# Kernel tuning notes

Measured on AMD Instinct MI355X. Metric: run time of the kernel, lower is better.

Reference implementation:

```python
import jax, jax.numpy as jnp
import numpy as np

NC = 10      # num_classes
HID = 64     # hidden_layer_dim
CIN = 512    # input_channels
THRESH = 100 # _LABEL2MASK_THRESHOL


def setup_inputs() -> dict:
    key = jax.random.key(0)
    k = jax.random.split(key, 5)
    B, h, w = 4, 60, 80
    feature1 = jax.random.normal(k[0], (B, CIN, h, w), jnp.float32)
    feature2 = jax.random.normal(k[1], (B, CIN, h // 2, w // 2), jnp.float32)
    s_in = (2.0 / CIN) ** 0.5   # kaiming_normal_ fan_in for 1x1 conv
    s_h = (2.0 / HID) ** 0.5
    w1 = jax.random.normal(k[2], (HID, CIN), jnp.float32) * s_in
    b1 = jnp.zeros((HID,), jnp.float32)
    w2 = jax.random.normal(k[3], (HID, CIN), jnp.float32) * s_in
    b2 = jnp.zeros((HID,), jnp.float32)
    w3 = jax.random.normal(k[4], (NC + 1, HID), jnp.float32) * s_h
    b3 = jnp.zeros((NC + 1,), jnp.float32)
    return {"feature1": feature1, "feature2": feature2,
            "w1": w1, "b1": b1, "w2": w2, "b2": b2, "w3": w3, "b3": b3}


def _resize_bilinear(x, H, W):
    # torch nn.Upsample(mode='bilinear', align_corners=False) ~ jax.image.resize bilinear
    B, C = x.shape[0], x.shape[1]
    return jax.image.resize(x, (B, C, H, W), method="bilinear")


def _label2bbx(seg):
    # Vectorized replacement of the batch x class Python loop: fused masked
    # min/max reductions per (batch, class). Classes 1..NC-1, class 0 skipped,
    # exactly as in the original. Fixed output shape (B*(NC-1), 6); rows with
    # pixel count < THRESH are filled with -1 (jit-compatible padding).
    B, H, W = seg.shape
    cls = jnp.arange(1, NC)                                   # (NC-1,)
    mask = seg[:, None, :, :] == cls[None, :, None, None]     # (B, NC-1, H, W)
    xs = jnp.arange(W)
    ys = jnp.arange(H)
    count = mask.sum(axis=(-2, -1))                           # (B, NC-1)
    xmin = jnp.min(jnp.where(mask, xs[None, None, None, :], W), axis=(-2, -1))
    xmax = jnp.max(jnp.where(mask, xs[None, None, None, :], -1), axis=(-2, -1))
    ymin = jnp.min(jnp.where(mask, ys[None, None, :, None], H), axis=(-2, -1))
    ymax = jnp.max(jnp.where(mask, ys[None, None, :, None], -1), axis=(-2, -1))
    bids = jnp.broadcast_to(jnp.arange(B)[:, None], (B, NC - 1))
    clsb = jnp.broadcast_to(cls[None, :], (B, NC - 1))
    bbx = jnp.stack([bids, xmin, ymin, xmax, ymax, clsb], axis=-1)  # (B, NC-1, 6)
    valid = (count >= THRESH)[..., None]
    return jnp.where(valid, bbx, -1).reshape(B * (NC - 1), 6)


def reference(feature1, feature2, w1, b1, w2, b2, w3, b3):
    # 1x1 convs expressed as channel GEMMs
    f1 = jax.nn.relu(jnp.einsum('bchw,oc->bohw', feature1, w1) + b1[None, :, None, None])
    f2 = jax.nn.relu(jnp.einsum('bchw,oc->bohw', feature2, w2) + b2[None, :, None, None])
    h, w = feature1.shape[2], feature1.shape[3]
    f2 = _resize_bilinear(f2, h, w)           # Upsample x2
    inter = f1 + f2
    up = _resize_bilinear(inter, 8 * h, 8 * w)  # Upsample x8
    logits = jax.nn.relu(jnp.einsum('bchw,oc->bohw', up, w3) + b3[None, :, None, None])
    probability = jax.nn.softmax(logits, axis=1)   # Softmax2d = softmax over C
    segmentation = jnp.argmax(probability, axis=1)  # (B, H, W)
    bbx = _label2bbx(segmentation)
    return probability, segmentation, bbx
```

## Files before the change

### kernel.cpp

```cpp
#include <hip/hip_runtime.h>

#define DEVINL __device__ __forceinline__

namespace {

constexpr int NB   = 4;
constexpr int CINv = 512;
constexpr int HIDv = 64;
constexpr int NCl  = 11;
constexpr int h1v = 60, w1v = 80;
constexpr int h2v = 30, w2v = 40;
constexpr int Hf = 480, Wf = 640;
constexpr int PPB1 = h1v * w1v;
constexpr int PPB2 = h2v * w2v;
constexpr int NP1 = NB * PPB1;
constexpr int NP2 = NB * PPB2;
constexpr int PPBF = Hf * Wf;
constexpr int NPF = NB * PPBF;

constexpr size_t WS_P1  = 0;
constexpr size_t WS_P2  = WS_P1 + 2ull * HIDv * NP1;
constexpr size_t WS_Z   = WS_P2 + 2ull * HIDv * NP2;
constexpr size_t WS_BBX = WS_Z + (size_t)NB * NCl * PPB1;

constexpr size_t OUT_SEG = (size_t)NB * NCl * PPBF;
constexpr size_t OUT_BBX = OUT_SEG + (size_t)NPF;

DEVINL int iclamp(int v, int lo, int hi) { return v < lo ? lo : (v > hi ? hi : v); }

template <int PPB>
DEVINL void gemm_tile(const float* __restrict__ F, const float* __restrict__ Wt,
                      float* __restrict__ P, int npix, int tile, int khalf,
                      float* A_lds , float* W_lds ) {
  const int t = threadIdx.x;
  const int pg = t & 15;
  const int og = t >> 4;
  const int gp0 = tile * 64;
  const int c0 = khalf * 256;

  float acc[4][4];
#pragma unroll
  for (int i = 0; i < 4; ++i)
#pragma unroll
    for (int j = 0; j < 4; ++j) acc[i][j] = 0.f;

  for (int kb = 0; kb < 8; ++kb) {
    const int cb = c0 + kb * 32;
    __syncthreads();
#pragma unroll
    for (int e = 0; e < 8; ++e) {
      int idx = e * 256 + t;
      int cc = idx >> 6, px = idx & 63;
      int gp = gp0 + px;
      int b = gp / PPB, pb = gp % PPB;
      A_lds[idx] = F[((size_t)b * CINv + (cb + cc)) * PPB + pb];
    }
#pragma unroll
    for (int e = 0; e < 8; ++e) {
      int idx = e * 256 + t;
      int o = idx >> 5, cc = idx & 31;
      W_lds[cc * 68 + o] = Wt[o * CINv + cb + cc];
    }
    __syncthreads();
#pragma unroll
    for (int cc = 0; cc < 32; ++cc) {
      float4 a = *reinterpret_cast<const float4*>(&A_lds[cc * 64 + pg * 4]);
      float4 w = *reinterpret_cast<const float4*>(&W_lds[cc * 68 + og * 4]);
      float av[4] = {a.x, a.y, a.z, a.w};
      float wv[4] = {w.x, w.y, w.z, w.w};
#pragma unroll
      for (int i = 0; i < 4; ++i)
#pragma unroll
        for (int j = 0; j < 4; ++j)
          acc[i][j] = fmaf(av[i], wv[j], acc[i][j]);
    }
  }
#pragma unroll
  for (int j = 0; j < 4; ++j) {
    int o = og * 4 + j;
    float4 v;
    v.x = acc[0][j]; v.y = acc[1][j]; v.z = acc[2][j]; v.w = acc[3][j];
    *reinterpret_cast<float4*>(&P[((size_t)khalf * HIDv + o) * npix + gp0 + pg * 4]) = v;
  }
}

__global__ __launch_bounds__(256) void k_gemm(const float* __restrict__ f1,
                                              const float* __restrict__ f2,
                                              const float* __restrict__ w1,
                                              const float* __restrict__ w2,
                                              float* __restrict__ ws) {
  __shared__ float A_lds[32 * 64];
  __shared__ float W_lds[32 * 68];
  const int bid = blockIdx.x;

  if (bid == 0 && threadIdx.x < 180) {
    int f = threadIdx.x % 5;
    int v = (f == 0) ? 0 : ((f == 1 || f == 3) ? 0x7fffffff : (int)0x80000000);
    reinterpret_cast<int*>(ws + WS_BBX)[threadIdx.x] = v;
  }

  if (bid < 600) {
    gemm_tile<PPB1>(f1, w1, ws + WS_P1, NP1, bid >> 1, bid & 1, A_lds, W_lds);
  } else {
    int tt = bid - 600;
    gemm_tile<PPB2>(f2, w2, ws + WS_P2, NP2, tt >> 1, tt & 1, A_lds, W_lds);
  }
}

__global__ __launch_bounds__(256) void k_combine_z(const float* __restrict__ ws_ro,
                                                   float* __restrict__ ws,
                                                   const float* __restrict__ b1,
                                                   const float* __restrict__ b2,
                                                   const float* __restrict__ w3,
                                                   const float* __restrict__ b3) {
  __shared__ float inter[64 * 64];
  const int t = threadIdx.x;
  const int pxl = t & 63;
  const int qi = t >> 6;
  const int gp = blockIdx.x * 64 + pxl;
  const int b = gp / PPB1, pb = gp % PPB1;
  const int y = pb / w1v, x = pb % w1v;

  const float sx = x * 0.5f - 0.25f;
  const float x0f = floorf(sx);
  const float fx = sx - x0f;
  const int ix0 = iclamp((int)x0f, 0, w2v - 1);
  const int ix1 = iclamp((int)x0f + 1, 0, w2v - 1);
  const float sy = y * 0.5f - 0.25f;
  const float y0f = floorf(sy);
  const float fy = sy - y0f;
  const int iy0 = iclamp((int)y0f, 0, h2v - 1);
  const int iy1 = iclamp((int)y0f + 1, 0, h2v - 1);

  const float* p1 = ws_ro + WS_P1;
  const float* p2 = ws_ro + WS_P2;
  const int base2 = b * PPB2;
  const int i00 = base2 + iy0 * w2v + ix0;
  const int i01 = base2 + iy0 * w2v + ix1;
  const int i10 = base2 + iy1 * w2v + ix0;
  const int i11 = base2 + iy1 * w2v + ix1;

#pragma unroll
  for (int cc = 0; cc < 16; ++cc) {
    const int ch = qi * 16 + cc;
    float v = p1[(size_t)ch * NP1 + gp] + p1[(size_t)(HIDv + ch) * NP1 + gp] + b1[ch];
    v = fmaxf(v, 0.f);
    const float* pa = p2 + (size_t)ch * NP2;
    const float* pbp = p2 + (size_t)(HIDv + ch) * NP2;
    const float bb = b2[ch];
    float v00 = fmaxf(pa[i00] + pbp[i00] + bb, 0.f);
    float v01 = fmaxf(pa[i01] + pbp[i01] + bb, 0.f);
    float v10 = fmaxf(pa[i10] + pbp[i10] + bb, 0.f);
    float v11 = fmaxf(pa[i11] + pbp[i11] + bb, 0.f);
    float top = v00 + fx * (v01 - v00);
    float bot = v10 + fx * (v11 - v10);
    v += top + fy * (bot - top);
    inter[ch * 64 + pxl] = v;
  }
  __syncthreads();

  const int o0 = qi * 3;
  const int ocnt = (qi == 3) ? 2 : 3;
  float* z = ws + WS_Z;
  for (int oo = 0; oo < ocnt; ++oo) {
    const int o = o0 + oo;
    float acc = b3[o];
#pragma unroll
    for (int ch = 0; ch < 64; ++ch)
      acc = fmaf(inter[ch * 64 + pxl], w3[o * HIDv + ch], acc);
    z[((size_t)b * NCl + o) * PPB1 + pb] = acc;
  }
}

__global__ __launch_bounds__(256) void k_up_softmax(const float* __restrict__ ws,
                                                    float* __restrict__ out,
                                                    int* __restrict__ bbxAcc) {
  constexpr int ZR = 3, ZC = 18, ZN = NCl * ZR * ZC;
  __shared__ float zt[ZN];
  __shared__ int sCnt[10], sXmin[10], sXmax[10], sYmin[10], sYmax[10];

  const int t = threadIdx.x;
  const int tile = blockIdx.x;
  const int tx = tile % 5;
  const int ty = (tile / 5) % 60;
  const int b  = tile / 300;

  const int base_x = tx * 16 - 1;
  const int base_y = ty - 1;

  if (t < 10) {
    sCnt[t] = 0;
    sXmin[t] = 0x7fffffff; sXmax[t] = (int)0x80000000;
    sYmin[t] = 0x7fffffff; sYmax[t] = (int)0x80000000;
  }
  const float* zb = ws + WS_Z + (size_t)b * NCl * PPB1;
  for (int e = t; e < ZN; e += 256) {
    int ch = e / (ZR * ZC);
    int rc = e % (ZR * ZC);
    int row = rc / ZC, col = rc % ZC;
    int gr = iclamp(base_y + row, 0, h1v - 1);
    int gc = iclamp(base_x + col, 0, w1v - 1);
    zt[e] = zb[(size_t)ch * PPB1 + gr * w1v + gc];
  }
  __syncthreads();

  const int xg = t & 31;
  const int yr = t >> 5;
  const int X = tx * 128 + xg * 4;
  const int Y = ty * 8 + yr;
  const int r = Y * Wf + X;

  const int lcx0 = (xg + 1) >> 1;
  const int lry0 = (yr >= 4) ? 1 : 0;
  const float fy = (Y + 0.5f) * 0.125f - 0.5f - (float)(base_y + lry0);
  float fxk[4];
#pragma unroll
  for (int k = 0; k < 4; ++k)
    fxk[k] = (X + k + 0.5f) * 0.125f - 0.5f - (float)(base_x + lcx0);

  float lg[NCl][4];
#pragma unroll
  for (int c = 0; c < NCl; ++c) {
    const int base = c * (ZR * ZC) + lry0 * ZC + lcx0;
    float v00 = zt[base],       v01 = zt[base + 1];
    float v10 = zt[base + ZC],  v11 = zt[base + ZC + 1];
    float l0 = v00 + fy * (v10 - v00);
    float l1 = v01 + fy * (v11 - v01);
#pragma unroll
    for (int k = 0; k < 4; ++k)
      lg[c][k] = fmaxf(l0 + fxk[k] * (l1 - l0), 0.f);
  }

  int bestc[4];
#pragma unroll
  for (int k = 0; k < 4; ++k) {
    float m = lg[0][k];
    int bi = 0;
#pragma unroll
    for (int c = 1; c < NCl; ++c) {
      if (lg[c][k] > m) { m = lg[c][k]; bi = c; }
    }
    bestc[k] = bi;
    float s = 0.f;
#pragma unroll
    for (int c = 0; c < NCl; ++c) {
      float e = __expf(lg[c][k] - m);
      lg[c][k] = e;
      s += e;
    }
    const float inv = __builtin_amdgcn_rcpf(s);
#pragma unroll
    for (int c = 0; c < NCl; ++c) lg[c][k] *= inv;
  }

  float* prob = out + (size_t)b * NCl * PPBF;
#pragma unroll
  for (int c = 0; c < NCl; ++c) {
    float4 v;
    v.x = lg[c][0]; v.y = lg[c][1]; v.z = lg[c][2]; v.w = lg[c][3];
    *reinterpret_cast<float4*>(&prob[(size_t)c * PPBF + r]) = v;
  }
  {
    float4 v;
    v.x = (float)bestc[0]; v.y = (float)bestc[1];
    v.z = (float)bestc[2]; v.w = (float)bestc[3];
    *reinterpret_cast<float4*>(&out[OUT_SEG + (size_t)b * PPBF + r]) = v;
  }

  for (int c = 1; c <= 9; ++c) {
    int cnt = 0, mnx = 0x7fffffff, mxx = (int)0x80000000;
#pragma unroll
    for (int k = 0; k < 4; ++k)
      if (bestc[k] == c) { ++cnt; mnx = min(mnx, X + k); mxx = max(mxx, X + k); }
    if (cnt) {
      atomicAdd(&sCnt[c], cnt);
      atomicMin(&sXmin[c], mnx);
      atomicMax(&sXmax[c], mxx);
      atomicMin(&sYmin[c], Y);
      atomicMax(&sYmax[c], Y);
    }
  }
  __syncthreads();
  if (t >= 1 && t <= 9 && sCnt[t] > 0) {
    int* e = bbxAcc + (b * 9 + (t - 1)) * 5;
    atomicAdd(e + 0, sCnt[t]);
    atomicMin(e + 1, sXmin[t]);
    atomicMax(e + 2, sXmax[t]);
    atomicMin(e + 3, sYmin[t]);
    atomicMax(e + 4, sYmax[t]);
  }
}

__global__ void k_bbx_final(const int* __restrict__ acc, float* __restrict__ out) {
  const int t = threadIdx.x;
  if (t >= 36) return;
  const int* e = acc + t * 5;
  float* o = out + OUT_BBX + t * 6;
  if (e[0] >= 100) {
    o[0] = (float)(t / 9);
    o[1] = (float)e[1];
    o[2] = (float)e[3];
    o[3] = (float)e[2];
    o[4] = (float)e[4];
    o[5] = (float)(t % 9 + 1);
  } else {
    for (int i = 0; i < 6; ++i) o[i] = -1.f;
  }
}

}

extern "C" void kernel_launch(void* const* d_in, const int* in_sizes, int n_in,
                              void* d_out, int out_size, void* d_ws, size_t ws_size,
                              hipStream_t stream) {
  const float* f1 = (const float*)d_in[0];
  const float* f2 = (const float*)d_in[1];
  const float* w1 = (const float*)d_in[2];
  const float* b1 = (const float*)d_in[3];
  const float* w2 = (const float*)d_in[4];
  const float* b2 = (const float*)d_in[5];
  const float* w3 = (const float*)d_in[6];
  const float* b3 = (const float*)d_in[7];
  float* out = (float*)d_out;
  float* ws = (float*)d_ws;

  hipLaunchKernelGGL(k_gemm, dim3(750), dim3(256), 0, stream, f1, f2, w1, w2, ws);
  hipLaunchKernelGGL(k_combine_z, dim3(300), dim3(256), 0, stream, ws, ws, b1, b2, w3, b3);
  hipLaunchKernelGGL(k_up_softmax, dim3(1200), dim3(256), 0, stream, ws, out,
                     (int*)(ws + WS_BBX));
  hipLaunchKernelGGL(k_bbx_final, dim3(1), dim3(64), 0, stream,
                     (const int*)(ws + WS_BBX), out);
}
```

Baseline: 86.09 us.

## Split bbox reduction into a ballot-based kernel and remap upsample-softmax to one pixel per thread

The upsample/softmax kernel drops its per-thread loop of shared-memory atomics for the bounding-box statistics. It now handles one pixel per thread over two output rows per block, using four times as many blocks and scalar coalesced stores. A new kernel rereads the segmentation map and computes per-class count and x/y extents with wavefront ballots, popcount and ctz/clz. The global accumulators are padded to a 32-int stride so different classes do not share a cache line. The cost is an extra kernel launch and a second read of the segmentation output.

```diff
diff --git a/kernel.cpp b/kernel.cpp
--- a/kernel.cpp
+++ b/kernel.cpp
@@ -94,9 +94,9 @@
   const int bid = blockIdx.x;
 
   if (bid == 0 && threadIdx.x < 180) {
-    int f = threadIdx.x % 5;
+    int entry = threadIdx.x / 5, f = threadIdx.x % 5;
     int v = (f == 0) ? 0 : ((f == 1 || f == 3) ? 0x7fffffff : (int)0x80000000);
-    reinterpret_cast<int*>(ws + WS_BBX)[threadIdx.x] = v;
+    reinterpret_cast<int*>(ws + WS_BBX)[entry * 32 + f] = v;
   }
 
   if (bid < 600) {
@@ -173,26 +173,18 @@
 }
 
 __global__ __launch_bounds__(256) void k_up_softmax(const float* __restrict__ ws,
-                                                    float* __restrict__ out,
-                                                    int* __restrict__ bbxAcc) {
+                                                    float* __restrict__ out) {
   constexpr int ZR = 3, ZC = 18, ZN = NCl * ZR * ZC;
   __shared__ float zt[ZN];
-  __shared__ int sCnt[10], sXmin[10], sXmax[10], sYmin[10], sYmax[10];
-
   const int t = threadIdx.x;
   const int tile = blockIdx.x;
   const int tx = tile % 5;
-  const int ty = (tile / 5) % 60;
-  const int b  = tile / 300;
-
+  const int ty = (tile / 5) % 240;
+  const int b  = tile / 1200;
   const int base_x = tx * 16 - 1;
-  const int base_y = ty - 1;
-
-  if (t < 10) {
-    sCnt[t] = 0;
-    sXmin[t] = 0x7fffffff; sXmax[t] = (int)0x80000000;
-    sYmin[t] = 0x7fffffff; sYmax[t] = (int)0x80000000;
-  }
+  const int row0 = ty * 2;
+  const int base_y = (int)floorf((row0 + 0.5f) * 0.125f - 0.5f);
+
   const float* zb = ws + WS_Z + (size_t)b * NCl * PPB1;
   for (int e = t; e < ZN; e += 256) {
     int ch = e / (ZR * ZC);
@@ -204,97 +196,110 @@
   }
   __syncthreads();
 
-  const int xg = t & 31;
-  const int yr = t >> 5;
-  const int X = tx * 128 + xg * 4;
-  const int Y = ty * 8 + yr;
-  const int r = Y * Wf + X;
-
-  const int lcx0 = (xg + 1) >> 1;
-  const int lry0 = (yr >= 4) ? 1 : 0;
-  const float fy = (Y + 0.5f) * 0.125f - 0.5f - (float)(base_y + lry0);
-  float fxk[4];
-#pragma unroll
-  for (int k = 0; k < 4; ++k)
-    fxk[k] = (X + k + 0.5f) * 0.125f - 0.5f - (float)(base_x + lcx0);
-
-  float lg[NCl][4];
+  const int x  = t & 127;
+  const int rr = t >> 7;
+  const int X = tx * 128 + x;
+  const int Y = row0 + rr;
+
+  const float sy = (Y + 0.5f) * 0.125f - 0.5f;
+  const int y0g = (int)floorf(sy);
+  const float fy = sy - (float)y0g;
+  const int lry = y0g - base_y;
+  const int lcx = (2 * x + 9) >> 4;
+  const float fx = (float)(2 * x - 7) * 0.0625f + 1.0f - (float)lcx;
+
+  float lg[NCl];
+  float m = -1.f;
+  int bi = 0;
 #pragma unroll
   for (int c = 0; c < NCl; ++c) {
-    const int base = c * (ZR * ZC) + lry0 * ZC + lcx0;
-    float v00 = zt[base],       v01 = zt[base + 1];
-    float v10 = zt[base + ZC],  v11 = zt[base + ZC + 1];
+    const int base = c * (ZR * ZC) + lry * ZC + lcx;
+    float v00 = zt[base],      v01 = zt[base + 1];
+    float v10 = zt[base + ZC], v11 = zt[base + ZC + 1];
     float l0 = v00 + fy * (v10 - v00);
     float l1 = v01 + fy * (v11 - v01);
-#pragma unroll
-    for (int k = 0; k < 4; ++k)
-      lg[c][k] = fmaxf(l0 + fxk[k] * (l1 - l0), 0.f);
-  }
-
-  int bestc[4];
-#pragma unroll
-  for (int k = 0; k < 4; ++k) {
-    float m = lg[0][k];
-    int bi = 0;
-#pragma unroll
-    for (int c = 1; c < NCl; ++c) {
-      if (lg[c][k] > m) { m = lg[c][k]; bi = c; }
-    }
-    bestc[k] = bi;
-    float s = 0.f;
-#pragma unroll
-    for (int c = 0; c < NCl; ++c) {
-      float e = __expf(lg[c][k] - m);
-      lg[c][k] = e;
-      s += e;
-    }
-    const float inv = __builtin_amdgcn_rcpf(s);
-#pragma unroll
-    for (int c = 0; c < NCl; ++c) lg[c][k] *= inv;
-  }
-
+    float v = fmaxf(l0 + fx * (l1 - l0), 0.f);
+    lg[c] = v;
+    if (v > m) { m = v; bi = c; }
+  }
+
+  float s = 0.f;
+#pragma unroll
+  for (int c = 0; c < NCl; ++c) {
+    float e = __expf(lg[c] - m);
+    lg[c] = e;
+    s += e;
+  }
+  const float inv = __builtin_amdgcn_rcpf(s);
+
+  const size_t r = (size_t)Y * Wf + X;
   float* prob = out + (size_t)b * NCl * PPBF;
 #pragma unroll
-  for (int c = 0; c < NCl; ++c) {
-    float4 v;
-    v.x = lg[c][0]; v.y = lg[c][1]; v.z = lg[c][2]; v.w = lg[c][3];
-    *reinterpret_cast<float4*>(&prob[(size_t)c * PPBF + r]) = v;
-  }
-  {
-    float4 v;
-    v.x = (float)bestc[0]; v.y = (float)bestc[1];
-    v.z = (float)bestc[2]; v.w = (float)bestc[3];
-    *reinterpret_cast<float4*>(&out[OUT_SEG + (size_t)b * PPBF + r]) = v;
-  }
-
-  for (int c = 1; c <= 9; ++c) {
-    int cnt = 0, mnx = 0x7fffffff, mxx = (int)0x80000000;
-#pragma unroll
-    for (int k = 0; k < 4; ++k)
-      if (bestc[k] == c) { ++cnt; mnx = min(mnx, X + k); mxx = max(mxx, X + k); }
-    if (cnt) {
-      atomicAdd(&sCnt[c], cnt);
-      atomicMin(&sXmin[c], mnx);
-      atomicMax(&sXmax[c], mxx);
-      atomicMin(&sYmin[c], Y);
-      atomicMax(&sYmax[c], Y);
-    }
+  for (int c = 0; c < NCl; ++c)
+    prob[(size_t)c * PPBF + r] = lg[c] * inv;
+  out[OUT_SEG + (size_t)b * PPBF + r] = (float)bi;
+}
+
+__global__ __launch_bounds__(256) void k_bbx(const float* __restrict__ seg,
+                                             int* __restrict__ acc) {
+  __shared__ int sC[10], sXn[10], sXx[10], sYn[10], sYx[10];
+  const int t = threadIdx.x;
+  const int lane = t & 63, w = t >> 6;
+  const int b = blockIdx.x / 120;
+  const int rg = blockIdx.x % 120;
+  const int row = rg * 4 + w;
+  if (t < 10) {
+    sC[t] = 0;
+    sXn[t] = 0x7fffffff; sXx[t] = (int)0x80000000;
+    sYn[t] = 0x7fffffff; sYx[t] = (int)0x80000000;
   }
   __syncthreads();
-  if (t >= 1 && t <= 9 && sCnt[t] > 0) {
-    int* e = bbxAcc + (b * 9 + (t - 1)) * 5;
-    atomicAdd(e + 0, sCnt[t]);
-    atomicMin(e + 1, sXmin[t]);
-    atomicMax(e + 2, sXmax[t]);
-    atomicMin(e + 3, sYmin[t]);
-    atomicMax(e + 4, sYmax[t]);
+
+  int cnt[10], xmn[10], xmx[10];
+#pragma unroll
+  for (int c = 1; c <= 9; ++c) { cnt[c] = 0; xmn[c] = 0x7fffffff; xmx[c] = -1; }
+
+  const float* srow = seg + (size_t)b * PPBF + (size_t)row * Wf;
+  for (int ch = 0; ch < 10; ++ch) {
+    const int cls = (int)srow[ch * 64 + lane];
+#pragma unroll
+    for (int c = 1; c <= 9; ++c) {
+      unsigned long long msk = __ballot(cls == c);
+      if (msk) {
+        cnt[c] += (int)__popcll(msk);
+        xmn[c] = min(xmn[c], ch * 64 + (int)__builtin_ctzll(msk));
+        xmx[c] = max(xmx[c], ch * 64 + 63 - (int)__builtin_clzll(msk));
+      }
+    }
+  }
+
+  if (lane == 0) {
+#pragma unroll
+    for (int c = 1; c <= 9; ++c) {
+      if (cnt[c]) {
+        atomicAdd(&sC[c], cnt[c]);
+        atomicMin(&sXn[c], xmn[c]);
+        atomicMax(&sXx[c], xmx[c]);
+        atomicMin(&sYn[c], row);
+        atomicMax(&sYx[c], row);
+      }
+    }
+  }
+  __syncthreads();
+  if (t >= 1 && t <= 9 && sC[t] > 0) {
+    int* e = acc + (b * 9 + (t - 1)) * 32;
+    atomicAdd(e + 0, sC[t]);
+    atomicMin(e + 1, sXn[t]);
+    atomicMax(e + 2, sXx[t]);
+    atomicMin(e + 3, sYn[t]);
+    atomicMax(e + 4, sYx[t]);
   }
 }
 
 __global__ void k_bbx_final(const int* __restrict__ acc, float* __restrict__ out) {
   const int t = threadIdx.x;
   if (t >= 36) return;
-  const int* e = acc + t * 5;
+  const int* e = acc + t * 32;
   float* o = out + OUT_BBX + t * 6;
   if (e[0] >= 100) {
     o[0] = (float)(t / 9);
@@ -326,7 +331,8 @@
 
   hipLaunchKernelGGL(k_gemm, dim3(750), dim3(256), 0, stream, f1, f2, w1, w2, ws);
   hipLaunchKernelGGL(k_combine_z, dim3(300), dim3(256), 0, stream, ws, ws, b1, b2, w3, b3);
-  hipLaunchKernelGGL(k_up_softmax, dim3(1200), dim3(256), 0, stream, ws, out,
+  hipLaunchKernelGGL(k_up_softmax, dim3(4800), dim3(256), 0, stream, ws, out);
+  hipLaunchKernelGGL(k_bbx, dim3(480), dim3(256), 0, stream, out + OUT_SEG,
                      (int*)(ws + WS_BBX));
   hipLaunchKernelGGL(k_bbx_final, dim3(1), dim3(64), 0, stream,
                      (const int*)(ws + WS_BBX), out);
```

Measured after the change: 69.48 us. 19.3% less time.
